# Kernel tuning notes

Hardware: AMD Instinct MI355X
Metric: run time of the kernel (lower is better)

Reference implementation:

```python
import jax, jax.numpy as jnp
import numpy as np
from jax import lax

MAXHD = 200.0
MAXV = 40.0
MINA = -6.0
MAXA = 4.0
DT = 0.1
PAST = 25
NVEH = 4096
NT = 256


def setup_inputs() -> dict:
    key = jax.random.key(0)
    ks = jax.random.split(key, 8)
    s = 0.1
    return dict(
        lead_states=jax.random.uniform(ks[0], (NVEH, NT + PAST - 1, 2), dtype=jnp.float32),
        cur_states=jax.random.uniform(ks[1], (NVEH, PAST, 2), dtype=jnp.float32),
        mask=jnp.ones((NVEH, NT + PAST - 1), dtype=jnp.float32),
        conv1_w=jax.random.normal(ks[2], (3, 3, 32), dtype=jnp.float32) * s,
        conv1_b=jnp.zeros((32,), dtype=jnp.float32),
        conv2_w=jax.random.normal(ks[3], (3, 32, 64), dtype=jnp.float32) * s,
        conv2_b=jnp.zeros((64,), dtype=jnp.float32),
        dense2_w=jax.random.normal(ks[4], (384, 10), dtype=jnp.float32) * s,
        dense2_b=jnp.zeros((10,), dtype=jnp.float32),
        dense1_w=jax.random.normal(ks[5], (10, 1), dtype=jnp.float32) * s,
        dense1_b=jnp.zeros((1,), dtype=jnp.float32),
        nt=NT,
    )


def reference(lead_states, cur_states, mask, conv1_w, conv1_b, conv2_w, conv2_b,
              dense2_w, dense2_b, dense1_w, dense1_b, nt):
    nveh = lead_states.shape[0]
    lead_pos = lead_states[:, :, 0]      # (nveh, nt+past-1)
    lead_speeds = lead_states[:, :, 1]

    dn = ('NWC', 'WIO', 'NWC')

    def cnn(x):
        # x: (nveh, PAST, 3)
        x = jax.nn.relu(lax.conv_general_dilated(x, conv1_w, (1,), 'SAME', dimension_numbers=dn) + conv1_b)
        x = lax.reduce_window(x, -jnp.inf, lax.max, (1, 2, 1), (1, 2, 1), 'SAME')   # (nveh,13,32)
        x = jax.nn.relu(lax.conv_general_dilated(x, conv2_w, (1,), 'VALID', dimension_numbers=dn) + conv2_b)
        x = lax.reduce_window(x, -jnp.inf, lax.max, (1, 2, 1), (1, 2, 1), 'SAME')   # (nveh,6,64)
        x = x.reshape(x.shape[0], -1)                                               # (nveh,384)
        x = jax.nn.relu(x @ dense2_w + dense2_b)
        x = x @ dense1_w + dense1_b                                                 # (nveh,1)
        return (MAXA - MINA) * x + MINA

    def step(carry, t):
        cur_pos, cur_speeds = carry                    # each (nveh, PAST)
        lp = lax.dynamic_slice(lead_pos, (0, t), (nveh, PAST))
        ls = lax.dynamic_slice(lead_speeds, (0, t), (nveh, PAST))
        x = jnp.stack([(lp - cur_pos) / MAXHD, cur_speeds / MAXV, ls / MAXV], axis=2)
        acc = cnn(x)                                   # (nveh,1)
        pred_pos = cur_pos[:, -1:] + DT * cur_speeds[:, -1:]
        pred_sp = cur_speeds[:, -1:] + DT * acc
        new_pos = jnp.concatenate([cur_pos[:, 1:], pred_pos], axis=1)
        new_sp = jnp.concatenate([cur_speeds[:, 1:], pred_sp], axis=1)
        return (new_pos, new_sp), (pred_pos[:, 0], pred_sp[:, 0])

    init = (cur_states[:, :, 0], cur_states[:, :, 1])
    _, (pos_preds, speed_preds) = lax.scan(step, init, jnp.arange(nt))
    # (nt, nveh) -> (nveh, nt, 2)
    return jnp.stack([pos_preds.T, speed_preds.T], axis=2)
```

## Files before the change

kernel.cpp:

```cpp
#include <hip/hip_runtime.h>
#include <stdint.h>


#define PAST 25
#define NTW_MAX 280

typedef __attribute__((ext_vector_type(8))) short bf16x8;
typedef __attribute__((ext_vector_type(4))) float f32x4;
typedef unsigned short u16x2 __attribute__((ext_vector_type(2)));
#define MFMA16 __builtin_amdgcn_mfma_f32_16x16x32_bf16

static __device__ __forceinline__ uint32_t f2bf(float f) {
  union { float f; uint32_t u; } x; x.f = f;
  return (x.u + 0x7FFFu + ((x.u >> 16) & 1u)) >> 16;
}
static __device__ __forceinline__ float bf2f(uint32_t b) {
  union { uint32_t u; float f; } x; x.u = b << 16; return x.f;
}
static __device__ __forceinline__ uint32_t pkbf(float lo, float hi) {
  uint32_t r;
  asm("v_cvt_pk_bf16_f32 %0, %1, %2" : "=v"(r) : "v"(lo), "v"(hi));
  return r;
}
static __device__ __forceinline__ f32x4 bcast4(float v) { f32x4 r = {v, v, v, v}; return r; }

static __device__ __forceinline__ uint32_t pkmax(uint32_t a, uint32_t b) {
#if __has_builtin(__builtin_elementwise_max)
  union U { uint32_t w; u16x2 v; } x, y; x.w = a; y.w = b;
  x.v = __builtin_elementwise_max(x.v, y.v);
  return x.w;
#else
  uint32_t al = a << 16, bl = b << 16;
  uint32_t lo = (al > bl ? al : bl) >> 16;
  uint32_t ah = a & 0xffff0000u, bh = b & 0xffff0000u;
  uint32_t hi = ah > bh ? ah : bh;
  return lo | hi;
#endif
}
static __device__ __forceinline__ uint4 maxq(uint4 a, uint4 b) {
  uint4 r; r.x = pkmax(a.x, b.x); r.y = pkmax(a.y, b.y);
  r.z = pkmax(a.z, b.z); r.w = pkmax(a.w, b.w); return r;
}
static __device__ __forceinline__ int w21(int x) { if (x >= 21) x -= 21; if (x >= 21) x -= 21; return x; }
static __device__ __forceinline__ int w17(int x) { if (x >= 17) x -= 17; if (x >= 17) x -= 17; return x; }
static __device__ __forceinline__ float rsum16(float x) {
  x += __builtin_bit_cast(float, __builtin_amdgcn_update_dpp(0, __builtin_bit_cast(int, x), 0x121, 0xf, 0xf, true));
  x += __builtin_bit_cast(float, __builtin_amdgcn_update_dpp(0, __builtin_bit_cast(int, x), 0x122, 0xf, 0xf, true));
  x += __builtin_bit_cast(float, __builtin_amdgcn_update_dpp(0, __builtin_bit_cast(int, x), 0x124, 0xf, 0xf, true));
  x += __builtin_bit_cast(float, __builtin_amdgcn_update_dpp(0, __builtin_bit_cast(int, x), 0x128, 0xf, 0xf, true));
  return x;
}

union FragU { bf16x8 v; uint16_t u[8]; uint4 q; };
struct RowD { f32x4 d0, d1; };

struct __align__(16) SMem {
  uint32_t Xcol[16][33][2];
  float    leadx[16][256];
  uint16_t leady[16][256];
  uint16_t P[25 * 16 * 32];
  uint16_t O2[22 * 16 * 64];
  float2 obuf[2][16][32];
  f32x4 JpartA[4][64];
  f32x4 JpartB[4][64];
};

__global__ __launch_bounds__(256, 1) void rnncf_kernel(
    const float* __restrict__ lead_states, const float* __restrict__ cur_states,
    const float* __restrict__ conv1_w, const float* __restrict__ conv1_b,
    const float* __restrict__ conv2_w, const float* __restrict__ conv2_b,
    const float* __restrict__ dense2_w, const float* __restrict__ dense2_b,
    const float* __restrict__ dense1_w, const float* __restrict__ dense1_b,
    float* __restrict__ out, int nt, int ntw) {
  __shared__ SMem sm;
  const int tid = threadIdx.x;
  const int lane = tid & 63;
  const int wid = tid >> 6;
  const int n = lane & 15;
  const int quad = lane >> 4;
  const int vbase = blockIdx.x * 16;

  for (int i = tid; i < 16 * PAST; i += 256) {
    int v = i & 15, u = i >> 4;
    const float2 l = *(const float2*)(lead_states + ((size_t)(vbase + v) * ntw + u) * 2);
    const float2 c = *(const float2*)(cur_states + ((size_t)(vbase + v) * PAST + u) * 2);
    float x0 = (l.x - c.x) * 0.005f;
    uint32_t w0 = pkbf(x0, c.y * 0.025f);
    sm.Xcol[v][u][0] = w0;
    sm.Xcol[v][u][1] = pkbf(l.y * 0.025f, x0 - bf2f(w0 & 0xffffu));
  }
#pragma unroll
  for (int v = 0; v < 16; ++v)
    for (int i = 25 + tid; i < ntw; i += 256) {
      const float2 l = *(const float2*)(lead_states + ((size_t)(vbase + v) * ntw + i) * 2);
      sm.leadx[v][i - 25] = l.x;
      sm.leady[v][i - 25] = (uint16_t)f2bf(l.y * 0.025f);
    }

  float pos_s = 0.f, spd_s = 0.f;
  if (wid == 3 && n < 4) {
    int veh = quad * 4 + n;
    const float2 c = *(const float2*)(cur_states + ((size_t)(vbase + veh) * PAST + 24) * 2);
    pos_s = c.x * 0.005f; spd_s = c.y * 0.025f;
  }

  FragU B1[2];
#pragma unroll
  for (int ct = 0; ct < 2; ++ct)
#pragma unroll
    for (int jj = 0; jj < 8; ++jj) {
      int k = quad * 8 + jj;
      int dw = k & 3, cig = (k >> 2) & 3;
      float w = 0.f;
      if (k < 16 && dw < 3) {
        int ci = (cig == 3) ? 0 : cig;
        w = conv1_w[(dw * 3 + ci) * 32 + ct * 16 + n];
      }
      B1[ct].u[jj] = (uint16_t)f2bf(w);
    }
  FragU B2[3][4];
#pragma unroll
  for (int dw = 0; dw < 3; ++dw)
#pragma unroll
    for (int ct = 0; ct < 4; ++ct)
#pragma unroll
      for (int jj = 0; jj < 8; ++jj) {
        int kap = quad * 8 + jj;
        int ci = (kap & 1) * 16 + (kap >> 1);
        B2[dw][ct].u[jj] = (uint16_t)f2bf(conv2_w[(dw * 32 + ci) * 64 + ct * 16 + n]);
      }
  FragU Bd[12];
#pragma unroll
  for (int kt = 0; kt < 12; ++kt)
#pragma unroll
    for (int jj = 0; jj < 8; ++jj) {
      int flat = kt * 32 + quad * 8 + jj;
      int jp = flat >> 6, kap = flat & 63;
      int co = (kap & 3) * 16 + (kap >> 2);
      Bd[kt].u[jj] = (uint16_t)f2bf((n < 10) ? dense2_w[(jp * 64 + co) * 10 + n] : 0.f);
    }
  f32x4 b1q0, b1q1;
#pragma unroll
  for (int r = 0; r < 4; ++r) {
    b1q0[r] = conv1_b[quad * 4 + r];
    b1q1[r] = conv1_b[16 + quad * 4 + r];
  }
  float b2v[4];
#pragma unroll
  for (int ct = 0; ct < 4; ++ct) b2v[ct] = conv2_b[ct * 16 + n];
  const float d2bv = (n < 10) ? dense2_b[n] : 0.f;
  const float wd1v = (n < 10) ? dense1_w[n] : 0.f;
  const float bd1v = dense1_b[0];

  auto pIdx = [&](int s, int veh, int ch) { return ((s * 16 + veh) * 4 + ch) * 8; };
  auto oIdx = [&](int s, int veh, int ch) { return ((s * 16 + veh) * 8 + ch) * 8; };

  auto build_x = [&](int c, int padL, int padR) -> FragU {
    int h = quad & 1, v8 = n;
    uint32_t d0 = padL ? 0u : sm.Xcol[v8][(c - 1) & 31][h];
    uint32_t d1 = sm.Xcol[v8][c & 31][h];
    uint32_t d2 = padR ? 0u : sm.Xcol[v8][(c + 1) & 31][h];
    FragU a;
    a.q.x = __builtin_amdgcn_perm(d1, d0, 0x05040100u);
    a.q.y = d2 & 0xffffu;
    a.q.z = __builtin_amdgcn_perm(d1, d0, 0x07060302u);
    a.q.w = d2 >> 16;
    return a;
  };

  auto conv1s_row = [&](int c, int padL, int padR) -> RowD {
    FragU a = build_x(c, padL, padR);
    RowD rd;
    rd.d0 = MFMA16(B1[0].v, a.v, b1q0, 0, 0, 0);
    rd.d1 = MFMA16(B1[1].v, a.v, b1q1, 0, 0, 0);
    return rd;
  };

  auto relumax4 = [&](const f32x4& a, const f32x4& b) -> f32x4 {
    f32x4 r;
#pragma unroll
    for (int i = 0; i < 4; ++i) r[i] = fmaxf(fmaxf(a[i], b[i]), 0.f);
    return r;
  };
  auto relu4 = [&](const f32x4& a) -> f32x4 {
    f32x4 r;
#pragma unroll
    for (int i = 0; i < 4; ++i) r[i] = fmaxf(a[i], 0.f);
    return r;
  };
  auto pack4 = [&](const f32x4& p0, const f32x4& p1) -> uint4 {
    uint4 w;
    w.x = pkbf(p0[0], p1[0]); w.y = pkbf(p0[1], p1[1]);
    w.z = pkbf(p0[2], p1[2]); w.w = pkbf(p0[3], p1[3]);
    return w;
  };
  auto p_store = [&](const uint4& w, int ds) {
    *(uint4*)&sm.P[pIdx(ds, n, quad ^ (n & 3))] = w;
  };
  auto pool_store = [&](const RowD& A, const RowD& Bq, int ds) {
    p_store(pack4(relumax4(A.d0, Bq.d0), relumax4(A.d1, Bq.d1)), ds);
  };

  auto ld_P = [&](int s) -> FragU {
    FragU a; a.q = *(const uint4*)&sm.P[pIdx(s, n, quad ^ (n & 3))]; return a;
  };

  auto conv2_acc = [&](f32x4* acc, int slot, int dw) {
    FragU a = ld_P(slot);
#pragma unroll
    for (int ct = 0; ct < 4; ++ct) acc[ct] = MFMA16(a.v, B2[dw][ct].v, acc[ct], 0, 0, 0);
  };

  auto conv2_accf = [&](f32x4* acc, const FragU& a, int dw) {
#pragma unroll
    for (int ct = 0; ct < 4; ++ct) acc[ct] = MFMA16(a.v, B2[dw][ct].v, acc[ct], 0, 0, 0);
  };

  auto o2_write = [&](const f32x4* acc, int ds) {
#pragma unroll
    for (int r = 0; r < 4; ++r) {
      int veh = quad * 4 + r;
      float m0 = fmaxf(acc[0][r], 0.f), m1 = fmaxf(acc[1][r], 0.f);
      float m2 = fmaxf(acc[2][r], 0.f), m3 = fmaxf(acc[3][r], 0.f);
      uint2 w2; w2.x = pkbf(m0, m1); w2.y = pkbf(m2, m3);
      *(uint2*)&sm.O2[oIdx(ds, veh, (n >> 1) ^ (veh & 7)) + (n & 1) * 4] = w2;
    }
  };

  auto dense_jp = [&](int pa, int pb, int jp, f32x4& a0, f32x4& a1) {
#pragma unroll
    for (int hf = 0; hf < 2; ++hf) {
      uint4 qa = *(const uint4*)&sm.O2[oIdx(pa, n, (hf * 4 + quad) ^ (n & 7))];
      if (pb >= 0) {
        uint4 qb = *(const uint4*)&sm.O2[oIdx(pb, n, (hf * 4 + quad) ^ (n & 7))];
        qa = maxq(qa, qb);
      }
      FragU a; a.q = qa;
      if (hf == 0) a0 = MFMA16(a.v, Bd[jp * 2].v, a0, 0, 0, 0);
      else         a1 = MFMA16(a.v, Bd[jp * 2 + 1].v, a1, 0, 0, 0);
    }
  };

  auto dense_jp_pre = [&](int pa, const uint4* qpre, int jp, f32x4& a0, f32x4& a1) {
#pragma unroll
    for (int hf = 0; hf < 2; ++hf) {
      uint4 qa = *(const uint4*)&sm.O2[oIdx(pa, n, (hf * 4 + quad) ^ (n & 7))];
      if (qpre) qa = maxq(qa, qpre[hf]);
      FragU a; a.q = qa;
      if (hf == 0) a0 = MFMA16(a.v, Bd[jp * 2].v, a0, 0, 0, 0);
      else         a1 = MFMA16(a.v, Bd[jp * 2 + 1].v, a1, 0, 0, 0);
    }
  };

  auto flush_out = [&](int bi, int t0, int cnt) {
    int vv = lane >> 2;
    int s0 = (lane & 3) * 8;
#pragma unroll
    for (int kk = 0; kk < 8; ++kk) {
      int s = s0 + kk;
      if (s < cnt) {
        float2 d = sm.obuf[bi][vv][s];
        *(float2*)(out + ((size_t)(vbase + vv) * nt + t0 + s) * 2) = d;
      }
    }
  };

  __syncthreads();

#pragma unroll
  for (int i = 0; i < 5; ++i) {
    int g = 2 + wid + 4 * i;
    RowD A = conv1s_row(g, 0, 0);
    RowD Bq = conv1s_row(g + 1, 0, 0);
    pool_store(A, Bq, g % 21);
  }
  __syncthreads();

#pragma unroll
  for (int i = 0; i < 4; ++i) {
    int a = 2 + wid + 4 * i;
    f32x4 acc[4];
#pragma unroll
    for (int ct = 0; ct < 4; ++ct) acc[ct] = bcast4(b2v[ct]);
    conv2_acc(acc, a % 21, 0);
    conv2_acc(acc, (a + 2) % 21, 1);
    conv2_acc(acc, (a + 4) % 21, 2);
    o2_write(acc, a % 17);
  }
  __syncthreads();

  RowD c1A = {};
  f32x4 accA[4] = {}, accB[4] = {};
  if (wid == 0) {
    RowD A = conv1s_row(0, 1, 0), Bq = conv1s_row(1, 0, 0);
    pool_store(A, Bq, 23);
  } else if (wid == 1) {
    RowD A = conv1s_row(1, 1, 0), Bq = conv1s_row(2, 0, 0);
    pool_store(A, Bq, 24);
  }
  __syncthreads();
  if (wid == 0) {
    f32x4 aj[4];
#pragma unroll
    for (int ct = 0; ct < 4; ++ct) aj[ct] = bcast4(b2v[ct]);
    conv2_acc(aj, 23, 0); conv2_acc(aj, 2, 1); conv2_acc(aj, 4, 2);
    o2_write(aj, 17);
  } else if (wid == 1) {
    f32x4 aj[4];
#pragma unroll
    for (int ct = 0; ct < 4; ++ct) aj[ct] = bcast4(b2v[ct]);
    conv2_acc(aj, 24, 0); conv2_acc(aj, 3, 1); conv2_acc(aj, 5, 2);
    o2_write(aj, 18);
  } else if (wid == 2) {
    RowD A = conv1s_row(4, 1, 0), Bq = conv1s_row(5, 0, 0);
    pool_store(A, Bq, 21);
  } else {
    RowD A = conv1s_row(5, 1, 0), Bq = conv1s_row(6, 0, 0);
    pool_store(A, Bq, 22);
  }
  __syncthreads();
  if (wid == 0) {
    f32x4 a0 = bcast4(d2bv), a1 = bcast4(0.f);
    dense_jp(17, 2, 0, a0, a1);
    dense_jp(4, 6, 1, a0, a1);
    dense_jp(8, 10, 2, a0, a1);
    dense_jp(12, 14, 3, a0, a1);
    sm.JpartA[0][lane] = a0; sm.JpartB[0][lane] = a1;
  } else if (wid == 1) {
    f32x4 a0 = bcast4(d2bv), a1 = bcast4(0.f);
    dense_jp(18, 3, 0, a0, a1);
    dense_jp(5, 7, 1, a0, a1);
    dense_jp(9, 11, 2, a0, a1);
    dense_jp(13, 15, 3, a0, a1);
    sm.JpartA[1][lane] = a0; sm.JpartB[1][lane] = a1;
  } else if (wid == 2) {
    RowD A = conv1s_row(2, 1, 0), Bq = conv1s_row(3, 0, 0);
    pool_store(A, Bq, 23);
  } else {
    RowD A = conv1s_row(3, 1, 0), Bq = conv1s_row(4, 0, 0);
    pool_store(A, Bq, 24);
  }
  __syncthreads();
  if (wid == 0) {
    f32x4 aj[4];
#pragma unroll
    for (int ct = 0; ct < 4; ++ct) aj[ct] = bcast4(b2v[ct]);
    conv2_acc(aj, 23, 0); conv2_acc(aj, 4, 1); conv2_acc(aj, 6, 2);
    o2_write(aj, 19);
  } else if (wid == 1) {
    f32x4 aj[4];
#pragma unroll
    for (int ct = 0; ct < 4; ++ct) aj[ct] = bcast4(b2v[ct]);
    conv2_acc(aj, 24, 0); conv2_acc(aj, 5, 1); conv2_acc(aj, 7, 2);
    o2_write(aj, 20);
  } else if (wid == 3) {
#pragma unroll
    for (int ct = 0; ct < 4; ++ct) accA[ct] = bcast4(b2v[ct]);
    conv2_acc(accA, 18, 0);
    conv2_acc(accA, 20, 1);
#pragma unroll
    for (int ct = 0; ct < 4; ++ct) accB[ct] = bcast4(b2v[ct]);
    conv2_acc(accB, 20, 0);
    c1A = conv1s_row(22, 0, 0);
  }
  __syncthreads();

  if (wid == 3) __builtin_amdgcn_s_setprio(2);

  int tmA21 = 0, tmA17 = 0;
  const int nsup = nt >> 1;
  for (int k = 0; k < nsup; ++k) {
    if (wid == 3) {
#pragma unroll
      for (int d = 0; d < 2; ++d) {
        const int t = 2 * k + d;
        const int sP22 = w21(tmA21 + d + 22);
        const int sO16 = w17(tmA17 + d + 16);
        const int sO18 = w17(tmA17 + d + 18);
        const int sP18n = w21(tmA21 + d + 19);
        const int sP20n = w21(tmA21 + d + 21);
        f32x4 jpA = sm.JpartA[t & 3][lane];
        f32x4 jpB = sm.JpartB[t & 3][lane];
        uint4 qj8[2];
#pragma unroll
        for (int hf = 0; hf < 2; ++hf)
          qj8[hf] = *(const uint4*)&sm.O2[oIdx(sO16, n, (hf * 4 + quad) ^ (n & 7))];
        FragU fA18 = ld_P(sP18n);
        FragU fA20 = ld_P(sP20n);
        RowD Bq = conv1s_row(t + 23, 0, 0);
        RowD Sg = conv1s_row(t + 24, 0, 1);
        uint4 w11 = pack4(relumax4(c1A.d0, Bq.d0), relumax4(c1A.d1, Bq.d1));
        uint4 w12 = pack4(relu4(Sg.d0), relu4(Sg.d1));
        p_store(w11, sP22);
        c1A = Bq;
        FragU f11; f11.q = w11;
        FragU f12; f12.q = w12;
        conv2_accf(accA, f11, 2);
        conv2_accf(accB, f11, 1);
        conv2_accf(accB, f12, 2);
        o2_write(accA, sO18);
        o2_write(accB, 21);
        f32x4 acc2 = bcast4(0.f), acc3 = bcast4(0.f);
        f32x4 acc4 = bcast4(0.f), acc5 = bcast4(0.f);
        dense_jp_pre(sO18, qj8, 4, acc2, acc3);
        dense_jp_pre(21, (const uint4*)nullptr, 5, acc4, acc5);
        float s0 = fmaxf(jpA[0] + jpB[0] + acc2[0] + acc3[0] + acc4[0] + acc5[0], 0.f) * wd1v;
        float s1 = fmaxf(jpA[1] + jpB[1] + acc2[1] + acc3[1] + acc4[1] + acc5[1], 0.f) * wd1v;
        float s2 = fmaxf(jpA[2] + jpB[2] + acc2[2] + acc3[2] + acc4[2] + acc5[2], 0.f) * wd1v;
        float s3 = fmaxf(jpA[3] + jpB[3] + acc2[3] + acc3[3] + acc4[3] + acc5[3], 0.f) * wd1v;
        s0 = rsum16(s0); s1 = rsum16(s1); s2 = rsum16(s2); s3 = rsum16(s3);
        if (n < 4) {
          int veh = quad * 4 + n;
          float sv = (n == 0) ? s0 : (n == 1) ? s1 : (n == 2) ? s2 : s3;
          float accv = 10.f * (sv + bd1v) - 6.f;
          float np_s = pos_s + 0.02f * spd_s;
          float nsp = spd_s * 40.f + 0.1f * accv;
          pos_s = np_s; spd_s = nsp * 0.025f;
          float2 o2v; o2v.x = np_s * 200.f; o2v.y = nsp;
          sm.obuf[(t >> 5) & 1][veh][t & 31] = o2v;
          int li = t; if (li > ntw - 26) li = ntw - 26;
          float lnx = sm.leadx[veh][li];
          float lny = bf2f(sm.leady[veh][li]);
          float x0 = lnx * 0.005f - np_s;
          uint32_t wlo = pkbf(x0, spd_s);
          sm.Xcol[veh][(t + PAST) & 31][0] = wlo;
          sm.Xcol[veh][(t + PAST) & 31][1] = pkbf(lny, x0 - bf2f(wlo & 0xffffu));
        }
#pragma unroll
        for (int ct = 0; ct < 4; ++ct) accA[ct] = bcast4(b2v[ct]);
        conv2_accf(accA, fA18, 0);
        conv2_accf(accA, fA20, 1);
#pragma unroll
        for (int ct = 0; ct < 4; ++ct) accB[ct] = bcast4(b2v[ct]);
        conv2_accf(accB, fA20, 0);
      }
    } else if (wid == 0) {
#pragma unroll
      for (int e = 0; e < 2; ++e) {
        const int tau = 2 * k + 2 + e;
        f32x4 a0 = bcast4(d2bv), a1 = bcast4(0.f);
        dense_jp(17 + (tau & 3), w17(tmA17 + 4 + e), 0, a0, a1);
        dense_jp(w17(tmA17 + 6 + e), w17(tmA17 + 8 + e), 1, a0, a1);
        dense_jp(w17(tmA17 + 10 + e), w17(tmA17 + 12 + e), 2, a0, a1);
        dense_jp(w17(tmA17 + 14 + e), w17(tmA17 + 16 + e), 3, a0, a1);
        sm.JpartA[tau & 3][lane] = a0;
        sm.JpartB[tau & 3][lane] = a1;
      }
    } else if (wid == 1) {
      if ((k & 15) == 0 && k > 0) {
        int t0 = 2 * k - 32;
        flush_out((t0 >> 5) & 1, t0, 32);
      }
#pragma unroll
      for (int e = 0; e < 2; ++e) {
        const int tau = 2 * k + 4 + e;
        f32x4 aj[4];
#pragma unroll
        for (int ct = 0; ct < 4; ++ct) aj[ct] = bcast4(b2v[ct]);
        conv2_acc(aj, 21 + (tau & 3), 0);
        conv2_acc(aj, w21(tmA21 + 6 + e), 1);
        conv2_acc(aj, w21(tmA21 + 8 + e), 2);
        o2_write(aj, 17 + (tau & 3));
      }
    } else {
#pragma unroll
      for (int f = 0; f < 2; ++f) {
        const int tau = 2 * k + 6 + f;
        RowD A = conv1s_row(tau, 1, 0);
        RowD Bq = conv1s_row(tau + 1, 0, 0);
        pool_store(A, Bq, 21 + (tau & 3));
      }
    }
    __syncthreads();
    tmA21 = w21(tmA21 + 2);
    tmA17 = w17(tmA17 + 2);
  }

  if (wid == 1) {
    int t0 = (nt - 1) & ~31;
    flush_out((t0 >> 5) & 1, t0, nt - t0);
  }
}

extern "C" void kernel_launch(void* const* d_in, const int* in_sizes, int n_in,
                              void* d_out, int out_size, void* d_ws, size_t ws_size,
                              hipStream_t stream) {
  const float* lead = (const float*)d_in[0];
  const float* cur  = (const float*)d_in[1];
  const float* c1w = (const float*)d_in[3];
  const float* c1b = (const float*)d_in[4];
  const float* c2w = (const float*)d_in[5];
  const float* c2b = (const float*)d_in[6];
  const float* d2w = (const float*)d_in[7];
  const float* d2b = (const float*)d_in[8];
  const float* d1w = (const float*)d_in[9];
  const float* d1b = (const float*)d_in[10];
  float* out = (float*)d_out;

  int nveh = in_sizes[1] / (PAST * 2);
  int ntw  = in_sizes[2] / nveh;
  int nt   = ntw - PAST + 1;
  int nblocks = nveh / 16;

  rnncf_kernel<<<nblocks, 256, 0, stream>>>(lead, cur, c1w, c1b, c2w, c2b,
                                            d2w, d2b, d1w, d1b, out, nt, ntw);
}
```

Baseline: 389.8 us.

## Offload conv2 partial sums from critical warp to helper warp via ring buffer

```diff
diff --git a/kernel.cpp b/kernel.cpp
--- a/kernel.cpp
+++ b/kernel.cpp
@@ -63,6 +63,8 @@
   float2 obuf[2][16][32];
   f32x4 JpartA[4][64];
   f32x4 JpartB[4][64];
+  f32x4 JA2[4][4][64];
+  f32x4 JB2[4][4][64];
 };
 
 __global__ __launch_bounds__(256, 1) void rnncf_kernel(
@@ -265,6 +267,20 @@
     }
   };
 
+  auto j9j10_partial = [&](int ring, int pA, int pB) {
+    f32x4 aA[4], aB[4];
+#pragma unroll
+    for (int ct = 0; ct < 4; ++ct) { aA[ct] = bcast4(b2v[ct]); aB[ct] = bcast4(b2v[ct]); }
+    conv2_acc(aA, pA, 0);
+    conv2_acc(aA, pB, 1);
+    conv2_acc(aB, pB, 0);
+#pragma unroll
+    for (int ct = 0; ct < 4; ++ct) {
+      sm.JA2[ring][ct][lane] = aA[ct];
+      sm.JB2[ring][ct][lane] = aB[ct];
+    }
+  };
+
   __syncthreads();
 
 #pragma unroll
@@ -290,7 +306,6 @@
   __syncthreads();
 
   RowD c1A = {};
-  f32x4 accA[4] = {}, accB[4] = {};
   if (wid == 0) {
     RowD A = conv1s_row(0, 1, 0), Bq = conv1s_row(1, 0, 0);
     pool_store(A, Bq, 23);
@@ -353,14 +368,10 @@
     for (int ct = 0; ct < 4; ++ct) aj[ct] = bcast4(b2v[ct]);
     conv2_acc(aj, 24, 0); conv2_acc(aj, 5, 1); conv2_acc(aj, 7, 2);
     o2_write(aj, 20);
-  } else if (wid == 3) {
-#pragma unroll
-    for (int ct = 0; ct < 4; ++ct) accA[ct] = bcast4(b2v[ct]);
-    conv2_acc(accA, 18, 0);
-    conv2_acc(accA, 20, 1);
-#pragma unroll
-    for (int ct = 0; ct < 4; ++ct) accB[ct] = bcast4(b2v[ct]);
-    conv2_acc(accB, 20, 0);
+  } else if (wid == 2) {
+    j9j10_partial(0, 18, 20);
+    j9j10_partial(1, 19, 0);
+  } else {
     c1A = conv1s_row(22, 0, 0);
   }
   __syncthreads();
@@ -377,29 +388,56 @@
         const int sP22 = w21(tmA21 + d + 22);
         const int sO16 = w17(tmA17 + d + 16);
         const int sO18 = w17(tmA17 + d + 18);
-        const int sP18n = w21(tmA21 + d + 19);
-        const int sP20n = w21(tmA21 + d + 21);
         f32x4 jpA = sm.JpartA[t & 3][lane];
         f32x4 jpB = sm.JpartB[t & 3][lane];
+        f32x4 pA[4], pB[4];
+#pragma unroll
+        for (int ct = 0; ct < 4; ++ct) {
+          pA[ct] = sm.JA2[t & 3][ct][lane];
+          pB[ct] = sm.JB2[t & 3][ct][lane];
+        }
         uint4 qj8[2];
 #pragma unroll
         for (int hf = 0; hf < 2; ++hf)
           qj8[hf] = *(const uint4*)&sm.O2[oIdx(sO16, n, (hf * 4 + quad) ^ (n & 7))];
-        FragU fA18 = ld_P(sP18n);
-        FragU fA20 = ld_P(sP20n);
-        RowD Bq = conv1s_row(t + 23, 0, 0);
-        RowD Sg = conv1s_row(t + 24, 0, 1);
-        uint4 w11 = pack4(relumax4(c1A.d0, Bq.d0), relumax4(c1A.d1, Bq.d1));
-        uint4 w12 = pack4(relu4(Sg.d0), relu4(Sg.d1));
-        p_store(w11, sP22);
-        c1A = Bq;
-        FragU f11; f11.q = w11;
-        FragU f12; f12.q = w12;
-        conv2_accf(accA, f11, 2);
-        conv2_accf(accB, f11, 1);
-        conv2_accf(accB, f12, 2);
-        o2_write(accA, sO18);
-        o2_write(accB, 21);
+        int li = t; if (li > ntw - 26) li = ntw - 26;
+        float lnx = 0.f, lny = 0.f;
+        if (n < 4) {
+          int veh = quad * 4 + n;
+          lnx = sm.leadx[veh][li];
+          lny = bf2f(sm.leady[veh][li]);
+        }
+        {
+          int h = quad & 1;
+          uint32_t d22 = sm.Xcol[n][(t + 22) & 31][h];
+          uint32_t d23 = sm.Xcol[n][(t + 23) & 31][h];
+          uint32_t d24 = sm.Xcol[n][(t + 24) & 31][h];
+          FragU aB, aS;
+          aB.q.x = __builtin_amdgcn_perm(d23, d22, 0x05040100u);
+          aB.q.y = d24 & 0xffffu;
+          aB.q.z = __builtin_amdgcn_perm(d23, d22, 0x07060302u);
+          aB.q.w = d24 >> 16;
+          aS.q.x = __builtin_amdgcn_perm(d24, d23, 0x05040100u);
+          aS.q.y = 0u;
+          aS.q.z = __builtin_amdgcn_perm(d24, d23, 0x07060302u);
+          aS.q.w = 0u;
+          RowD Bq, Sg;
+          Bq.d0 = MFMA16(B1[0].v, aB.v, b1q0, 0, 0, 0);
+          Bq.d1 = MFMA16(B1[1].v, aB.v, b1q1, 0, 0, 0);
+          Sg.d0 = MFMA16(B1[0].v, aS.v, b1q0, 0, 0, 0);
+          Sg.d1 = MFMA16(B1[1].v, aS.v, b1q1, 0, 0, 0);
+          uint4 w11 = pack4(relumax4(c1A.d0, Bq.d0), relumax4(c1A.d1, Bq.d1));
+          uint4 w12 = pack4(relu4(Sg.d0), relu4(Sg.d1));
+          p_store(w11, sP22);
+          c1A = Bq;
+          FragU f11; f11.q = w11;
+          FragU f12; f12.q = w12;
+          conv2_accf(pA, f11, 2);
+          conv2_accf(pB, f11, 1);
+          conv2_accf(pB, f12, 2);
+          o2_write(pA, sO18);
+          o2_write(pB, 21);
+        }
         f32x4 acc2 = bcast4(0.f), acc3 = bcast4(0.f);
         f32x4 acc4 = bcast4(0.f), acc5 = bcast4(0.f);
         dense_jp_pre(sO18, qj8, 4, acc2, acc3);
@@ -418,21 +456,11 @@
           pos_s = np_s; spd_s = nsp * 0.025f;
           float2 o2v; o2v.x = np_s * 200.f; o2v.y = nsp;
           sm.obuf[(t >> 5) & 1][veh][t & 31] = o2v;
-          int li = t; if (li > ntw - 26) li = ntw - 26;
-          float lnx = sm.leadx[veh][li];
-          float lny = bf2f(sm.leady[veh][li]);
           float x0 = lnx * 0.005f - np_s;
           uint32_t wlo = pkbf(x0, spd_s);
           sm.Xcol[veh][(t + PAST) & 31][0] = wlo;
           sm.Xcol[veh][(t + PAST) & 31][1] = pkbf(lny, x0 - bf2f(wlo & 0xffffu));
         }
-#pragma unroll
-        for (int ct = 0; ct < 4; ++ct) accA[ct] = bcast4(b2v[ct]);
-        conv2_accf(accA, fA18, 0);
-        conv2_accf(accA, fA20, 1);
-#pragma unroll
-        for (int ct = 0; ct < 4; ++ct) accB[ct] = bcast4(b2v[ct]);
-        conv2_accf(accB, fA20, 0);
       }
     } else if (wid == 0) {
 #pragma unroll
@@ -463,6 +491,11 @@
         o2_write(aj, 17 + (tau & 3));
       }
     } else {
+#pragma unroll
+      for (int e = 0; e < 2; ++e) {
+        const int tau = 2 * k + 2 + e;
+        j9j10_partial(tau & 3, w21(tmA21 + 20 + e), w21(tmA21 + 22 + e));
+      }
 #pragma unroll
       for (int f = 0; f < 2; ++f) {
         const int tau = 2 * k + 6 + f;
```

Result: faster. 351.7 us (-9.8%).
